# Performance work log

Measured on AMD Instinct MI355X. Metric: run time of the kernel, lower is better.

Reference implementation:

```python
import jax, jax.numpy as jnp
import numpy as np

V = 32000        # vocab_size
OOV = 100        # max_oovs
VT = V + OOV
E = 256          # embed_size
H = 256          # hidden_size
PAD_INDEX = 0


def _gru_cell(x, h, w_ih, w_hh, b_ih, b_hh):
    # PyTorch GRU gate order: r, z, n
    gi = x @ w_ih.T + b_ih
    gh = h @ w_hh.T + b_hh
    ir, iz, inn = jnp.split(gi, 3, axis=-1)
    hr, hz, hn = jnp.split(gh, 3, axis=-1)
    r = jax.nn.sigmoid(ir + hr)
    z = jax.nn.sigmoid(iz + hz)
    n = jnp.tanh(inn + r * hn)
    return (1.0 - z) * n + z * h


def setup_inputs() -> dict:
    key = jax.random.key(0)
    ks = jax.random.split(key, 16)
    bs, max_len, seq_len = 32, 64, 128
    inputs = jax.random.randint(ks[0], (bs, max_len), 0, V, dtype=jnp.int32)
    encoded = jax.random.normal(ks[1], (bs, seq_len, 2 * H), dtype=jnp.float32)
    encoded_idx = jax.random.randint(ks[2], (bs, seq_len), 0, VT, dtype=jnp.int32)
    s = 0.02
    return {
        "inputs": inputs,
        "encoded": encoded,
        "encoded_idx": encoded_idx,
        "bridge_w": s * jax.random.normal(ks[3], (H, 2 * H), dtype=jnp.float32),
        "embed": s * jax.random.normal(ks[4], (V, E), dtype=jnp.float32),
        "gru_w_ih": s * jax.random.normal(ks[5], (3 * H, E + 2 * H), dtype=jnp.float32),
        "gru_w_hh": s * jax.random.normal(ks[6], (3 * H, H), dtype=jnp.float32),
        "gru_b_ih": jnp.zeros((3 * H,), dtype=jnp.float32),
        "gru_b_hh": jnp.zeros((3 * H,), dtype=jnp.float32),
        "Wg_w": s * jax.random.normal(ks[7], (V, H), dtype=jnp.float32),
        "Wg_b": jnp.zeros((V,), dtype=jnp.float32),
        "Wo_w": s * jax.random.normal(ks[8], (H, 2 * H), dtype=jnp.float32),
        "Wo_b": jnp.zeros((H,), dtype=jnp.float32),
    }


def decoder_forward(inputs, encoded, encoded_idx, bridge_w, embed,
                    gru_w_ih, gru_w_hh, gru_b_ih, gru_b_hh,
                    Wg_w, Wg_b, Wo_w, Wo_b):
    bs, seq_len, _ = encoded.shape
    # precomputed per-sequence quantities (as in original forward())
    enc_scores = jnp.tanh(encoded @ Wo_w.T + Wo_b)            # [bs, seq, H]
    pad_mask = jnp.where(encoded_idx == PAD_INDEX, -1000.0, 0.0)  # [bs, seq]
    b_idx = jnp.arange(bs)[:, None]

    s0 = encoded[:, -1, :] @ bridge_w.T                        # [bs, H]
    ctx0 = jnp.zeros((bs, 2 * H), dtype=encoded.dtype)

    def step(carry, inp):
        s_prev, ctx = carry
        x = embed[inp]                                         # [bs, E]
        gru_in = jnp.concatenate([x, ctx], axis=-1)            # [bs, E+2H]
        s_t = _gru_cell(gru_in, s_prev, gru_w_ih, gru_w_hh, gru_b_ih, gru_b_hh)
        psi_g = s_t @ Wg_w.T + Wg_b                            # [bs, V]
        psi_c = jnp.einsum('bsh,bh->bs', enc_scores, s_t) + pad_mask
        p = jax.nn.softmax(jnp.concatenate([psi_g, psi_c], axis=1), axis=1)
        prob_g = jnp.concatenate(
            [p[:, :V], jnp.full((bs, OOV), 1e-4, dtype=p.dtype)], axis=1)  # [bs, VT]
        prob_c = p[:, V:]                                      # [bs, seq]
        # scatter-add of copy probs onto extended vocab (one-hot bmm in original)
        prob_c_to_g = jnp.zeros((bs, VT), dtype=p.dtype).at[b_idx, encoded_idx].add(prob_c)
        out = prob_g + prob_c_to_g                             # [bs, VT]
        # selective read: reweight copy probs at positions matching current input
        rel = (encoded_idx == inp[:, None]).astype(p.dtype)
        cw = rel * prob_c
        cw = cw / jnp.maximum(cw.sum(axis=1, keepdims=True), 1e-12)  # F.normalize p=1
        new_ctx = jnp.einsum('bs,bsd->bd', cw, encoded)        # [bs, 2H]
        return (s_t, new_ctx), out

    (_, _), outs = jax.lax.scan(step, (s0, ctx0), inputs.T)    # [max_len, bs, VT]
    return jnp.transpose(outs, (1, 0, 2))                      # [bs, max_len, VT]


def reference(inputs, encoded, encoded_idx, bridge_w, embed,
              gru_w_ih, gru_w_hh, gru_b_ih, gru_b_hh,
              Wg_w, Wg_b, Wo_w, Wo_b):
    return decoder_forward(inputs, encoded, encoded_idx, bridge_w, embed,
                           gru_w_ih, gru_w_hh, gru_b_ih, gru_b_hh,
                           Wg_w, Wg_b, Wo_w, Wo_b)
```

## Files before the change

### kernel.cpp

```cpp
#include <hip/hip_runtime.h>
#include <math.h>
#include <stdint.h>

static const int VOC  = 32000;
static const int VT_  = 32100;

typedef __attribute__((ext_vector_type(8))) short bf16x8_t;
typedef __attribute__((ext_vector_type(4))) float f32x4_t;

__device__ __forceinline__ unsigned short f2bf(float f) {
  union { float f; unsigned int u; } v; v.f = f;
  unsigned int u = v.u;
  u = u + 0x7FFFu + ((u >> 16) & 1u);
  return (unsigned short)(u >> 16);
}
__device__ __forceinline__ float bf2f(unsigned short u) {
  union { unsigned int i; float f; } w; w.i = ((unsigned int)u) << 16; return w.f;
}
__device__ __forceinline__ float bfbits(unsigned int u) {
  union { unsigned int i; float f; } w; w.i = u; return w.f;
}
__device__ __forceinline__ int nth_set(unsigned long long m0, unsigned long long m1, int j) {
  int c0 = __popcll(m0);
  unsigned long long m = m0; int base = 0;
  if (j >= c0) { j -= c0; m = m1; base = 64; }
  for (int k = 0; k < j; k++) m &= m - 1;
  return base + (__ffsll((long long)m) - 1);
}

__global__ __launch_bounds__(256) void k_pre0(
    const float* __restrict__ wg, unsigned short* __restrict__ WG16,
    const float* __restrict__ whh, unsigned short* __restrict__ WHH16,
    const float* __restrict__ enc, unsigned short* __restrict__ EH,
    unsigned short* __restrict__ EL,
    const float* __restrict__ wo, unsigned short* __restrict__ WOH,
    unsigned short* __restrict__ WOL,
    const float* __restrict__ wih, unsigned short* __restrict__ WIH16,
    const float* __restrict__ embed, const int* __restrict__ inputs,
    unsigned short* __restrict__ X16) {
  int q = blockIdx.x, tid = threadIdx.x;
  if (q < 1024) {
    for (int i = q * 256 + tid; i < 2048000; i += 1024 * 256) {
      float4 f = ((const float4*)wg)[i];
      ushort4 o;
      o.x = f2bf(f.x); o.y = f2bf(f.y); o.z = f2bf(f.z); o.w = f2bf(f.w);
      ((ushort4*)WG16)[i] = o;
    }
  } else if (q < 1036) {
    for (int i = (q - 1024) * 256 + tid; i < 49152; i += 12 * 256) {
      float4 f = ((const float4*)whh)[i];
      ushort4 o;
      o.x = f2bf(f.x); o.y = f2bf(f.y); o.z = f2bf(f.z); o.w = f2bf(f.w);
      ((ushort4*)WHH16)[i] = o;
    }
  } else if (q < 1292) {
    for (int i = (q - 1036) * 256 + tid; i < 524288; i += 256 * 256) {
      float4 f = ((const float4*)enc)[i];
      ushort4 h, l;
      h.x = f2bf(f.x); l.x = f2bf(f.x - bf2f(h.x));
      h.y = f2bf(f.y); l.y = f2bf(f.y - bf2f(h.y));
      h.z = f2bf(f.z); l.z = f2bf(f.z - bf2f(h.z));
      h.w = f2bf(f.w); l.w = f2bf(f.w - bf2f(h.w));
      ((ushort4*)EH)[i] = h;
      ((ushort4*)EL)[i] = l;
    }
  } else if (q < 1300) {
    for (int i = (q - 1292) * 256 + tid; i < 32768; i += 8 * 256) {
      float4 f = ((const float4*)wo)[i];
      ushort4 h, l;
      h.x = f2bf(f.x); l.x = f2bf(f.x - bf2f(h.x));
      h.y = f2bf(f.y); l.y = f2bf(f.y - bf2f(h.y));
      h.z = f2bf(f.z); l.z = f2bf(f.z - bf2f(h.z));
      h.w = f2bf(f.w); l.w = f2bf(f.w - bf2f(h.w));
      ((ushort4*)WOH)[i] = h;
      ((ushort4*)WOL)[i] = l;
    }
  } else if (q < 1312) {
    for (int g = (q - 1300) * 256 + tid; g < 49152; g += 12 * 256) {
      int row = g >> 6, col = g & 63;
      float4 f = ((const float4*)(wih + (size_t)row * 768))[col];
      ushort4 o;
      o.x = f2bf(f.x); o.y = f2bf(f.y); o.z = f2bf(f.z); o.w = f2bf(f.w);
      ((ushort4*)X16)[0];
      ((ushort4*)WIH16)[g] = o;
    }
  } else {
    for (int g = (q - 1312) * 256 + tid; g < 131072; g += 128 * 256) {
      int r = g >> 6, col = g & 63;
      float4 f = ((const float4*)(embed + (size_t)inputs[r] * 256))[col];
      ushort4 o;
      o.x = f2bf(f.x); o.y = f2bf(f.y); o.z = f2bf(f.z); o.w = f2bf(f.w);
      ((ushort4*)X16)[g] = o;
    }
  }
}

__global__ __launch_bounds__(256) void k_pre1(
    const unsigned short* __restrict__ EH, const unsigned short* __restrict__ EL,
    const unsigned short* __restrict__ WOH, const unsigned short* __restrict__ WOL,
    const float* __restrict__ wob, float* __restrict__ ENCSC,
    const unsigned short* __restrict__ X16, const unsigned short* __restrict__ WIH16,
    const float* __restrict__ bih, float* __restrict__ XG,
    const float* __restrict__ enc, const float* __restrict__ bridge,
    float* __restrict__ S0,
    const float* __restrict__ wih, const int* __restrict__ encidx,
    const int* __restrict__ inputs, float* __restrict__ ENCIH) {
  __shared__ int flag;
  int q = blockIdx.x, tid = threadIdx.x;
  int wid = tid >> 6, lane = tid & 63;
  int wm = wid >> 1, wn = wid & 1;
  int quad = lane >> 4, l15 = lane & 15;
  if (q < 256) {
    int bm = q >> 2, bn = q & 3;
    int r0 = bm * 64 + wm * 32, n0 = bn * 64 + wn * 32;
    f32x4_t acc[2][2];
#pragma unroll
    for (int i = 0; i < 2; i++)
#pragma unroll
      for (int j = 0; j < 2; j++) acc[i][j] = (f32x4_t){0.f, 0.f, 0.f, 0.f};
    for (int kc = 0; kc < 16; kc++) {
      int ko = kc * 32 + quad * 8;
      bf16x8_t ah[2], al[2], bh[2], bl[2];
#pragma unroll
      for (int i = 0; i < 2; i++) {
        size_t off = (size_t)(r0 + i * 16 + l15) * 512 + ko;
        ah[i] = *(const bf16x8_t*)(EH + off);
        al[i] = *(const bf16x8_t*)(EL + off);
      }
#pragma unroll
      for (int j = 0; j < 2; j++) {
        size_t off = (size_t)(n0 + j * 16 + l15) * 512 + ko;
        bh[j] = *(const bf16x8_t*)(WOH + off);
        bl[j] = *(const bf16x8_t*)(WOL + off);
      }
#pragma unroll
      for (int i = 0; i < 2; i++)
#pragma unroll
        for (int j = 0; j < 2; j++) {
          acc[i][j] = __builtin_amdgcn_mfma_f32_16x16x32_bf16(ah[i], bh[j], acc[i][j], 0, 0, 0);
          acc[i][j] = __builtin_amdgcn_mfma_f32_16x16x32_bf16(ah[i], bl[j], acc[i][j], 0, 0, 0);
          acc[i][j] = __builtin_amdgcn_mfma_f32_16x16x32_bf16(al[i], bh[j], acc[i][j], 0, 0, 0);
        }
    }
#pragma unroll
    for (int i = 0; i < 2; i++)
#pragma unroll
      for (int j = 0; j < 2; j++)
#pragma unroll
        for (int p = 0; p < 4; p++) {
          int row = r0 + i * 16 + quad * 4 + p;
          int col = n0 + j * 16 + l15;
          ENCSC[(size_t)row * 256 + col] = tanhf(acc[i][j][p] + wob[col]);
        }
  } else if (q < 640) {
    int p2 = q - 256;
    int bm = p2 & 31, bn = p2 >> 5;
    int r0 = bm * 64 + wm * 32, n0 = bn * 64 + wn * 32;
    f32x4_t acc[2][2];
#pragma unroll
    for (int i = 0; i < 2; i++)
#pragma unroll
      for (int j = 0; j < 2; j++) acc[i][j] = (f32x4_t){0.f, 0.f, 0.f, 0.f};
    for (int kc = 0; kc < 8; kc++) {
      int ko = kc * 32 + quad * 8;
      bf16x8_t a[2], b[2];
#pragma unroll
      for (int i = 0; i < 2; i++)
        a[i] = *(const bf16x8_t*)(X16 + (size_t)(r0 + i * 16 + l15) * 256 + ko);
#pragma unroll
      for (int j = 0; j < 2; j++)
        b[j] = *(const bf16x8_t*)(WIH16 + (size_t)(n0 + j * 16 + l15) * 256 + ko);
#pragma unroll
      for (int i = 0; i < 2; i++)
#pragma unroll
        for (int j = 0; j < 2; j++)
          acc[i][j] = __builtin_amdgcn_mfma_f32_16x16x32_bf16(a[i], b[j], acc[i][j], 0, 0, 0);
    }
#pragma unroll
    for (int i = 0; i < 2; i++)
#pragma unroll
      for (int j = 0; j < 2; j++)
#pragma unroll
        for (int p = 0; p < 4; p++) {
          int row = r0 + i * 16 + quad * 4 + p;
          int col = n0 + j * 16 + l15;
          XG[(size_t)row * 768 + col] = acc[i][j][p] + bih[col];
        }
  } else if (q < 672) {
    int b = q - 640, h = tid;
    const float4* a4 = (const float4*)(enc + ((size_t)b * 128 + 127) * 512);
    const float4* w4 = (const float4*)(bridge + (size_t)h * 512);
    float acc = 0.f;
    for (int k = 0; k < 128; k++) {
      float4 a = a4[k], w = w4[k];
      acc += a.x * w.x + a.y * w.y + a.z * w.z + a.w * w.w;
    }
    S0[b * 256 + h] = acc;
  } else {
    int bs = q - 672;
    int b = bs >> 7;
    int idx = encidx[bs];
    if (tid < 64) {
      unsigned long long m = __ballot(inputs[b * 64 + tid] == idx);
      if (tid == 0) flag = (m != 0ULL);
    }
    __syncthreads();
    if (!flag) return;
    const float4* e4 = (const float4*)(enc + (size_t)bs * 512);
    for (int d = tid; d < 768; d += 256) {
      const float4* w4 = (const float4*)(wih + (size_t)d * 768 + 256);
      float acc = 0.f;
      for (int k = 0; k < 128; k++) {
        float4 e = e4[k], w = w4[k];
        acc += e.x * w.x + e.y * w.y + e.z * w.z + e.w * w.w;
      }
      ENCIH[(size_t)bs * 768 + d] = acc;
    }
  }
}

__global__ __launch_bounds__(768, 1) void k_seq(
    const unsigned short* __restrict__ whb,
    const float* __restrict__ bhh,
    const float* __restrict__ xg, const float* __restrict__ encsc,
    const float* __restrict__ encih, const int* __restrict__ encidx,
    const int* __restrict__ inputs, const float* __restrict__ s0,
    float* __restrict__ S32, unsigned short* __restrict__ S16) {
  __shared__ float sbuf[256];
  __shared__ __align__(16) unsigned short sb16[256];
  __shared__ float ghp[768];
  __shared__ float psis[128];
  __shared__ int eidx_sh[128];
  __shared__ int inp_sh[64];
  __shared__ unsigned long long mmask[64][2];
  __shared__ __align__(16) unsigned short wlds[73728];
  int b = blockIdx.x;
  int tid = threadIdx.x;
  int wid = tid >> 6, lane = tid & 63;
  int quad = lane >> 4, l15 = lane & 15;
  int n0 = wid * 64;
  int h = tid;
#pragma unroll
  for (int c = 0; c < 4; c++)
#pragma unroll
    for (int kt2 = 0; kt2 < 3; kt2++) {
      int4 v = *(const int4*)(whb + (size_t)(n0 + c * 16 + l15) * 256 + 160 + kt2 * 32 + quad * 8);
      *(int4*)(wlds + wid * 6144 + (c * 3 + kt2) * 512 + (l15 * 4 + quad) * 8) = v;
    }
  bf16x8_t wf[20];
#pragma unroll
  for (int c = 0; c < 4; c++)
#pragma unroll
    for (int kt = 0; kt < 5; kt++)
      wf[c * 5 + kt] = *(const bf16x8_t*)(whb + (size_t)(n0 + c * 16 + l15) * 256 + kt * 32 + quad * 8);
  float bR = 0.f, bZ = 0.f, bN = 0.f, ctxR = 0.f, ctxZ = 0.f, ctxN = 0.f;
  if (tid < 256) {
    bR = bhh[h]; bZ = bhh[256 + h]; bN = bhh[512 + h];
    float v = s0[b * 256 + tid];
    sbuf[tid] = v;
    sb16[tid] = f2bf(v);
  }
  if (tid < 128) eidx_sh[tid] = encidx[b * 128 + tid];
  if (tid < 64) inp_sh[tid] = inputs[b * 64 + tid];
  __syncthreads();
  if (tid < 128) {
    int e = eidx_sh[tid];
    for (int t = 0; t < 64; t++) {
      unsigned long long bal = __ballot(e == inp_sh[t]);
      if (lane == 0) mmask[t][wid] = bal;
    }
  }
  __syncthreads();
  for (int t = 0; t < 64; t++) {
    int r = b * 64 + t;
    float xr0 = 0.f, xr1 = 0.f, xr2 = 0.f;
    if (tid < 256) {
      const float* xr = xg + (size_t)r * 768;
      xr0 = xr[h]; xr1 = xr[256 + h]; xr2 = xr[512 + h];
    }
    f32x4_t a0 = {0.f,0.f,0.f,0.f}, a1 = {0.f,0.f,0.f,0.f};
    f32x4_t a2 = {0.f,0.f,0.f,0.f}, a3 = {0.f,0.f,0.f,0.f};
#pragma unroll
    for (int kt = 0; kt < 5; kt++) {
      bf16x8_t af = *(const bf16x8_t*)(sb16 + kt * 32 + quad * 8);
      a0 = __builtin_amdgcn_mfma_f32_16x16x32_bf16(af, wf[ 0 + kt], a0, 0, 0, 0);
      a1 = __builtin_amdgcn_mfma_f32_16x16x32_bf16(af, wf[ 5 + kt], a1, 0, 0, 0);
      a2 = __builtin_amdgcn_mfma_f32_16x16x32_bf16(af, wf[10 + kt], a2, 0, 0, 0);
      a3 = __builtin_amdgcn_mfma_f32_16x16x32_bf16(af, wf[15 + kt], a3, 0, 0, 0);
    }
#pragma unroll
    for (int kt2 = 0; kt2 < 3; kt2++) {
      bf16x8_t af = *(const bf16x8_t*)(sb16 + (5 + kt2) * 32 + quad * 8);
      const unsigned short* wb = wlds + wid * 6144 + kt2 * 512 + (l15 * 4 + quad) * 8;
      a0 = __builtin_amdgcn_mfma_f32_16x16x32_bf16(af, *(const bf16x8_t*)(wb +    0), a0, 0, 0, 0);
      a1 = __builtin_amdgcn_mfma_f32_16x16x32_bf16(af, *(const bf16x8_t*)(wb + 1536), a1, 0, 0, 0);
      a2 = __builtin_amdgcn_mfma_f32_16x16x32_bf16(af, *(const bf16x8_t*)(wb + 3072), a2, 0, 0, 0);
      a3 = __builtin_amdgcn_mfma_f32_16x16x32_bf16(af, *(const bf16x8_t*)(wb + 4608), a3, 0, 0, 0);
    }
    if (lane < 16) {
      ghp[n0 +      lane] = a0[0];
      ghp[n0 + 16 + lane] = a1[0];
      ghp[n0 + 32 + lane] = a2[0];
      ghp[n0 + 48 + lane] = a3[0];
    }
    __syncthreads();
    if (tid < 256) {
      float hr = ghp[h] + bR;
      float hz = ghp[256 + h] + bZ;
      float hn = ghp[512 + h] + bN;
      float gr = xr0 + ctxR;
      float gz = xr1 + ctxZ;
      float gn = xr2 + ctxN;
      float rgate = 1.f / (1.f + expf(-(gr + hr)));
      float zgate = 1.f / (1.f + expf(-(gz + hz)));
      float ngate = tanhf(gn + rgate * hn);
      float sold = sbuf[h];
      float snew = (1.f - zgate) * ngate + zgate * sold;
      unsigned short u16 = f2bf(snew);
      S32[(size_t)r * 256 + h] = snew;
      S16[(size_t)r * 256 + h] = u16;
      sbuf[h] = snew;
      sb16[h] = u16;
    }
    __syncthreads();
    if (t == 63) break;
    unsigned long long m0 = mmask[t][0], m1 = mmask[t][1];
    int mc = __popcll(m0) + __popcll(m1);
    if (mc > 0) {
      for (int j = wid; j < mc; j += 12) {
        int s = nth_set(m0, m1, j);
        const float4* e4 = (const float4*)(encsc + (size_t)(b * 128 + s) * 256);
        float4 ev = e4[lane];
        float4 sv = ((const float4*)sbuf)[lane];
        float v = ev.x * sv.x + ev.y * sv.y + ev.z * sv.z + ev.w * sv.w;
#pragma unroll
        for (int off = 32; off >= 1; off >>= 1) v += __shfl_down(v, off);
        if (lane == 0) psis[j] = v + (eidx_sh[s] == 0 ? -1000.f : 0.f);
      }
      __syncthreads();
      if (tid == 0) {
        float mx = -3e38f;
        for (int j = 0; j < mc; j++) mx = fmaxf(mx, psis[j]);
        if (mx < -500.f) {
          for (int j = 0; j < mc; j++) psis[j] = 0.f;
        } else {
          float ss = 0.f;
          for (int j = 0; j < mc; j++) { float e = expf(psis[j] - mx); psis[j] = e; ss += e; }
          float rs = 1.f / ss;
          for (int j = 0; j < mc; j++) psis[j] *= rs;
        }
      }
      __syncthreads();
      if (tid < 256) {
        ctxR = 0.f; ctxZ = 0.f; ctxN = 0.f;
        unsigned long long mm0 = m0, mm1 = m1;
        for (int j = 0; j < mc; j++) {
          int s;
          if (mm0) { s = __ffsll((long long)mm0) - 1; mm0 &= mm0 - 1; }
          else     { s = 64 + __ffsll((long long)mm1) - 1; mm1 &= mm1 - 1; }
          float c = psis[j];
          const float* e = encih + (size_t)(b * 128 + s) * 768;
          ctxR += c * e[h]; ctxZ += c * e[256 + h]; ctxN += c * e[512 + h];
        }
      }
    } else if (tid < 256) {
      ctxR = 0.f; ctxZ = 0.f; ctxN = 0.f;
    }
  }
}

__global__ __launch_bounds__(256) void k_mid(const unsigned short* __restrict__ S16,
                                             const unsigned short* __restrict__ WG16,
                                             const float* __restrict__ wgb,
                                             unsigned short* __restrict__ pe16,
                                             const float* __restrict__ S32,
                                             const float* __restrict__ encsc,
                                             const int* __restrict__ encidx,
                                             float* __restrict__ psic) {
  int q = blockIdx.x;
  int tid = threadIdx.x;
  if (q >= 250) {
    int q2 = q - 250;
    int b = q2 >> 1, ny = q2 & 1;
    int ti = tid & 15, tj = tid >> 4;
    int r0 = b * 64 + ti * 4;
    int s0 = ny * 64 + tj * 4;
    const float4* A[4]; const float4* B[4];
#pragma unroll
    for (int i = 0; i < 4; i++) A[i] = (const float4*)(S32 + (size_t)(r0 + i) * 256);
#pragma unroll
    for (int j = 0; j < 4; j++) B[j] = (const float4*)(encsc + (size_t)(b * 128 + s0 + j) * 256);
    float acc[4][4];
#pragma unroll
    for (int i = 0; i < 4; i++)
#pragma unroll
      for (int j = 0; j < 4; j++) acc[i][j] = 0.f;
    for (int k = 0; k < 64; k++) {
      float4 a[4], bb[4];
#pragma unroll
      for (int i = 0; i < 4; i++) a[i] = A[i][k];
#pragma unroll
      for (int j = 0; j < 4; j++) bb[j] = B[j][k];
#pragma unroll
      for (int i = 0; i < 4; i++)
#pragma unroll
        for (int j = 0; j < 4; j++)
          acc[i][j] += a[i].x * bb[j].x + a[i].y * bb[j].y + a[i].z * bb[j].z + a[i].w * bb[j].w;
    }
#pragma unroll
    for (int i = 0; i < 4; i++)
#pragma unroll
      for (int j = 0; j < 4; j++) {
        float v = acc[i][j] + (encidx[b * 128 + s0 + j] == 0 ? -1000.f : 0.f);
        psic[(size_t)(r0 + i) * 128 + s0 + j] = v;
      }
    return;
  }
  __shared__ unsigned short lB[128 * 256];
  __shared__ unsigned short lA[128 * 256];
  int nc = q;
  int wid = tid >> 6, lane = tid & 63;
  int wm = wid >> 1, wn = wid & 1;
  int quad = lane >> 4, l15 = lane & 15;
#pragma unroll
  for (int u = 0; u < 16; u++) {
    int c = u * 256 + tid;
    int row = c >> 5, ch = c & 31;
    int sch = (ch & 24) | ((ch & 7) ^ (row & 7));
    __builtin_amdgcn_global_load_lds(
        (const __attribute__((address_space(1))) unsigned int*)(WG16 + (size_t)(nc * 128 + row) * 256 + sch * 8),
        (__attribute__((address_space(3))) unsigned int*)(lB + c * 8), 16, 0, 0);
  }
  float bj[4];
#pragma unroll
  for (int j = 0; j < 4; j++) bj[j] = wgb[nc * 128 + wn * 64 + j * 16 + l15];
  for (int mt = 0; mt < 16; mt++) {
#pragma unroll
    for (int u = 0; u < 16; u++) {
      int c = u * 256 + tid;
      int row = c >> 5, ch = c & 31;
      int sch = (ch & 24) | ((ch & 7) ^ (row & 7));
      __builtin_amdgcn_global_load_lds(
          (const __attribute__((address_space(1))) unsigned int*)(S16 + (size_t)(mt * 128 + row) * 256 + sch * 8),
          (__attribute__((address_space(3))) unsigned int*)(lA + c * 8), 16, 0, 0);
    }
    __syncthreads();
    f32x4_t acc[4][4];
#pragma unroll
    for (int i = 0; i < 4; i++)
#pragma unroll
      for (int j = 0; j < 4; j++) acc[i][j] = (f32x4_t){0.f, 0.f, 0.f, 0.f};
#pragma unroll
    for (int kc = 0; kc < 8; kc++) {
      int g = kc * 4 + quad;
      int slotoff = ((g & 24) | ((g & 7) ^ (l15 & 7))) * 8;
      bf16x8_t af[4], bfr[4];
#pragma unroll
      for (int i = 0; i < 4; i++)
        af[i] = *(const bf16x8_t*)(lA + (wm * 64 + i * 16 + l15) * 256 + slotoff);
#pragma unroll
      for (int j = 0; j < 4; j++)
        bfr[j] = *(const bf16x8_t*)(lB + (wn * 64 + j * 16 + l15) * 256 + slotoff);
#pragma unroll
      for (int i = 0; i < 4; i++)
#pragma unroll
        for (int j = 0; j < 4; j++)
          acc[i][j] = __builtin_amdgcn_mfma_f32_16x16x32_bf16(af[i], bfr[j], acc[i][j], 0, 0, 0);
    }
#pragma unroll
    for (int i = 0; i < 4; i++)
#pragma unroll
      for (int p = 0; p < 4; p++) {
        int rg = mt * 128 + wm * 64 + i * 16 + quad * 4 + p;
        size_t base = (size_t)rg * 32000 + nc * 128 + wn * 64 + l15;
#pragma unroll
        for (int j = 0; j < 4; j++)
          pe16[base + j * 16] = f2bf(expf(acc[i][j][p] + bj[j]));
      }
    __syncthreads();
  }
}

__global__ __launch_bounds__(256) void k_pb(const unsigned short* __restrict__ pe16,
                                            const float* __restrict__ psic,
                                            const int* __restrict__ encidx,
                                            float* __restrict__ outp) {
  __shared__ float red[8];
  int r = blockIdx.x;
  int b = r >> 6;
  int tid = threadIdx.x;
  int wid = tid >> 6, lane = tid & 63;
  const unsigned short* prow = pe16 + (size_t)r * 32000;
  float* orow = outp + (size_t)r * VT_;
  int4 ev[16];
#pragma unroll
  for (int u = 0; u < 16; u++) {
    int c8 = u * 256 + tid;
    if (c8 < 4000) ev[u] = *(const int4*)(prow + c8 * 8);
    else ev[u] = (int4){0, 0, 0, 0};
  }
  float sumE = 0.f;
#pragma unroll
  for (int u = 0; u < 16; u++) {
    unsigned int xs0 = (unsigned int)ev[u].x, xs1 = (unsigned int)ev[u].y;
    unsigned int xs2 = (unsigned int)ev[u].z, xs3 = (unsigned int)ev[u].w;
    sumE += bfbits(xs0 << 16) + bfbits(xs0 & 0xffff0000u);
    sumE += bfbits(xs1 << 16) + bfbits(xs1 & 0xffff0000u);
    sumE += bfbits(xs2 << 16) + bfbits(xs2 & 0xffff0000u);
    sumE += bfbits(xs3 << 16) + bfbits(xs3 & 0xffff0000u);
  }
  float t = sumE;
#pragma unroll
  for (int off = 32; off >= 1; off >>= 1) t += __shfl_xor(t, off);
  if (lane == 0) red[wid] = t;
  float pc = (tid < 128) ? psic[(size_t)r * 128 + tid] : -3e38f;
  float mv = pc;
#pragma unroll
  for (int off = 32; off >= 1; off >>= 1) mv = fmaxf(mv, __shfl_xor(mv, off));
  if (lane == 0) red[4 + wid] = mv;
  __syncthreads();
  float sumEt = red[0] + red[1] + red[2] + red[3];
  float Mc = fmaxf(fmaxf(red[4], red[5]), fmaxf(red[6], red[7]));
  float D = fmaxf(Mc - 30.f, 0.f);
  float w = expf(-D);
  __syncthreads();
  float ec = (tid < 128) ? expf(pc - D) : 0.f;
  float zt = ec;
#pragma unroll
  for (int off = 32; off >= 1; off >>= 1) zt += __shfl_xor(zt, off);
  if (lane == 0) red[wid] = zt;
  __syncthreads();
  float Z = w * sumEt + (red[0] + red[1] + red[2] + red[3]);
  float gs = w / Z;
#pragma unroll 2
  for (int u = 0; u < 16; u++) {
    int c8 = u * 256 + tid;
    if (c8 < 4000) {
      int c0 = c8 * 8;
      unsigned int xs0 = (unsigned int)ev[u].x, xs1 = (unsigned int)ev[u].y;
      unsigned int xs2 = (unsigned int)ev[u].z, xs3 = (unsigned int)ev[u].w;
      float4 o0, o1;
      o0.x = bfbits(xs0 << 16) * gs;         o0.y = bfbits(xs0 & 0xffff0000u) * gs;
      o0.z = bfbits(xs1 << 16) * gs;         o0.w = bfbits(xs1 & 0xffff0000u) * gs;
      o1.x = bfbits(xs2 << 16) * gs;         o1.y = bfbits(xs2 & 0xffff0000u) * gs;
      o1.z = bfbits(xs3 << 16) * gs;         o1.w = bfbits(xs3 & 0xffff0000u) * gs;
      *(float4*)(orow + c0) = o0;
      *(float4*)(orow + c0 + 4) = o1;
    }
  }
  if (tid < 100) orow[32000 + tid] = 1e-4f;
  __syncthreads();
  if (tid < 128) {
    int idx = encidx[b * 128 + tid];
    atomicAdd(&orow[idx], ec / Z);
  }
}

extern "C" void kernel_launch(void* const* d_in, const int* in_sizes, int n_in,
                              void* d_out, int out_size, void* d_ws, size_t ws_size,
                              hipStream_t stream) {
  (void)in_sizes; (void)n_in; (void)out_size; (void)ws_size;
  const int*   inputs  = (const int*)d_in[0];
  const float* encoded = (const float*)d_in[1];
  const int*   encidx  = (const int*)d_in[2];
  const float* bridge  = (const float*)d_in[3];
  const float* embed   = (const float*)d_in[4];
  const float* wih     = (const float*)d_in[5];
  const float* whh     = (const float*)d_in[6];
  const float* bih     = (const float*)d_in[7];
  const float* bhh     = (const float*)d_in[8];
  const float* wg      = (const float*)d_in[9];
  const float* wgb     = (const float*)d_in[10];
  const float* wo      = (const float*)d_in[11];
  const float* wob     = (const float*)d_in[12];
  float* out = (float*)d_out;

  char* ws = (char*)d_ws;
  size_t off = 0;
  auto alloc = [&](size_t bytes) -> void* {
    void* p = ws + off;
    off += (bytes + 255) & ~(size_t)255;
    return p;
  };
  unsigned short* WG16  = (unsigned short*)alloc((size_t)32000 * 256 * 2);
  unsigned short* WHH16 = (unsigned short*)alloc((size_t)768 * 256 * 2);
  unsigned short* EH    = (unsigned short*)alloc((size_t)4096 * 512 * 2);
  unsigned short* EL    = (unsigned short*)alloc((size_t)4096 * 512 * 2);
  unsigned short* WOH   = (unsigned short*)alloc((size_t)256 * 512 * 2);
  unsigned short* WOL   = (unsigned short*)alloc((size_t)256 * 512 * 2);
  unsigned short* WIH16 = (unsigned short*)alloc((size_t)768 * 256 * 2);
  unsigned short* X16   = (unsigned short*)alloc((size_t)2048 * 256 * 2);
  float* S32            = (float*)alloc((size_t)2048 * 256 * 4);
  unsigned short* S16   = (unsigned short*)alloc((size_t)2048 * 256 * 2);
  float* ENCSC          = (float*)alloc((size_t)4096 * 256 * 4);
  float* ENCIH          = (float*)alloc((size_t)4096 * 768 * 4);
  float* XG             = (float*)alloc((size_t)2048 * 768 * 4);
  float* S0             = (float*)alloc((size_t)32 * 256 * 4);
  float* PSIC           = (float*)alloc((size_t)2048 * 128 * 4);
  unsigned short* PE16  = (unsigned short*)alloc((size_t)2048 * 32000 * 2);

  k_pre0<<<1440, 256, 0, stream>>>(wg, WG16, whh, WHH16, encoded, EH, EL,
                                   wo, WOH, WOL, wih, WIH16, embed, inputs, X16);
  k_pre1<<<4768, 256, 0, stream>>>(EH, EL, WOH, WOL, wob, ENCSC,
                                   X16, WIH16, bih, XG,
                                   encoded, bridge, S0, wih, encidx, inputs, ENCIH);
  k_seq<<<32, 768, 0, stream>>>(WHH16, bhh, XG, ENCSC, ENCIH, encidx, inputs, S0, S32, S16);
  k_mid<<<314, 256, 0, stream>>>(S16, WG16, wgb, PE16, S32, ENCSC, encidx, PSIC);
  k_pb<<<2048, 256, 0, stream>>>(PE16, PSIC, encidx, out);
}
```

Baseline: 776.2 us.

## Fuse softmax row-sum partials into vocab GEMM epilogue, drop register-held row in k_pb

The vocab projection kernel now sums the bf16-rounded exp values per row tile with cross-lane shuffles and shared memory, and writes per-(row, column-block) partial sums to a new buffer. The normalisation kernel reduces those 250 partials instead of reading and summing the whole 32000-entry bf16 row before the scaling pass. It then loads the row only once, inside the scale loop, so the 16 int4 values no longer have to be held in registers. This adds shuffles, one shared-memory write and a block barrier per tile in the GEMM epilogue, plus a small extra global buffer.

```diff
diff --git a/kernel.cpp b/kernel.cpp
--- a/kernel.cpp
+++ b/kernel.cpp
@@ -81,7 +81,6 @@
       float4 f = ((const float4*)(wih + (size_t)row * 768))[col];
       ushort4 o;
       o.x = f2bf(f.x); o.y = f2bf(f.y); o.z = f2bf(f.z); o.w = f2bf(f.w);
-      ((ushort4*)X16)[0];
       ((ushort4*)WIH16)[g] = o;
     }
   } else {
@@ -373,6 +372,7 @@
                                              const unsigned short* __restrict__ WG16,
                                              const float* __restrict__ wgb,
                                              unsigned short* __restrict__ pe16,
+                                             float* __restrict__ psum,
                                              const float* __restrict__ S32,
                                              const float* __restrict__ encsc,
                                              const int* __restrict__ encidx,
@@ -418,6 +418,7 @@
   }
   __shared__ unsigned short lB[128 * 256];
   __shared__ unsigned short lA[128 * 256];
+  __shared__ float zpart[2][128];
   int nc = q;
   int wid = tid >> 6, lane = tid & 63;
   int wm = wid >> 1, wn = wid & 1;
@@ -471,17 +472,28 @@
     for (int i = 0; i < 4; i++)
 #pragma unroll
       for (int p = 0; p < 4; p++) {
-        int rg = mt * 128 + wm * 64 + i * 16 + quad * 4 + p;
+        int rl = wm * 64 + i * 16 + quad * 4 + p;
+        int rg = mt * 128 + rl;
         size_t base = (size_t)rg * 32000 + nc * 128 + wn * 64 + l15;
-#pragma unroll
-        for (int j = 0; j < 4; j++)
-          pe16[base + j * 16] = f2bf(expf(acc[i][j][p] + bj[j]));
+        float rs = 0.f;
+#pragma unroll
+        for (int j = 0; j < 4; j++) {
+          unsigned short us = f2bf(expf(acc[i][j][p] + bj[j]));
+          pe16[base + j * 16] = us;
+          rs += bf2f(us);
+        }
+#pragma unroll
+        for (int off = 1; off < 16; off <<= 1) rs += __shfl_xor(rs, off);
+        if (l15 == 0) zpart[wn][rl] = rs;
       }
     __syncthreads();
+    if (tid < 128)
+      psum[(size_t)(mt * 128 + tid) * 256 + nc] = zpart[0][tid] + zpart[1][tid];
   }
 }
 
 __global__ __launch_bounds__(256) void k_pb(const unsigned short* __restrict__ pe16,
+                                            const float* __restrict__ psum,
                                             const float* __restrict__ psic,
                                             const int* __restrict__ encidx,
                                             float* __restrict__ outp) {
@@ -492,27 +504,10 @@
   int wid = tid >> 6, lane = tid & 63;
   const unsigned short* prow = pe16 + (size_t)r * 32000;
   float* orow = outp + (size_t)r * VT_;
-  int4 ev[16];
-#pragma unroll
-  for (int u = 0; u < 16; u++) {
-    int c8 = u * 256 + tid;
-    if (c8 < 4000) ev[u] = *(const int4*)(prow + c8 * 8);
-    else ev[u] = (int4){0, 0, 0, 0};
-  }
-  float sumE = 0.f;
-#pragma unroll
-  for (int u = 0; u < 16; u++) {
-    unsigned int xs0 = (unsigned int)ev[u].x, xs1 = (unsigned int)ev[u].y;
-    unsigned int xs2 = (unsigned int)ev[u].z, xs3 = (unsigned int)ev[u].w;
-    sumE += bfbits(xs0 << 16) + bfbits(xs0 & 0xffff0000u);
-    sumE += bfbits(xs1 << 16) + bfbits(xs1 & 0xffff0000u);
-    sumE += bfbits(xs2 << 16) + bfbits(xs2 & 0xffff0000u);
-    sumE += bfbits(xs3 << 16) + bfbits(xs3 & 0xffff0000u);
-  }
-  float t = sumE;
-#pragma unroll
-  for (int off = 32; off >= 1; off >>= 1) t += __shfl_xor(t, off);
-  if (lane == 0) red[wid] = t;
+  float zp = (tid < 250) ? psum[(size_t)r * 256 + tid] : 0.f;
+#pragma unroll
+  for (int off = 32; off >= 1; off >>= 1) zp += __shfl_xor(zp, off);
+  if (lane == 0) red[wid] = zp;
   float pc = (tid < 128) ? psic[(size_t)r * 128 + tid] : -3e38f;
   float mv = pc;
 #pragma unroll
@@ -532,13 +527,13 @@
   __syncthreads();
   float Z = w * sumEt + (red[0] + red[1] + red[2] + red[3]);
   float gs = w / Z;
-#pragma unroll 2
   for (int u = 0; u < 16; u++) {
     int c8 = u * 256 + tid;
     if (c8 < 4000) {
       int c0 = c8 * 8;
-      unsigned int xs0 = (unsigned int)ev[u].x, xs1 = (unsigned int)ev[u].y;
-      unsigned int xs2 = (unsigned int)ev[u].z, xs3 = (unsigned int)ev[u].w;
+      int4 v = *(const int4*)(prow + c0);
+      unsigned int xs0 = (unsigned int)v.x, xs1 = (unsigned int)v.y;
+      unsigned int xs2 = (unsigned int)v.z, xs3 = (unsigned int)v.w;
       float4 o0, o1;
       o0.x = bfbits(xs0 << 16) * gs;         o0.y = bfbits(xs0 & 0xffff0000u) * gs;
       o0.z = bfbits(xs1 << 16) * gs;         o0.w = bfbits(xs1 & 0xffff0000u) * gs;
@@ -597,6 +592,7 @@
   float* XG             = (float*)alloc((size_t)2048 * 768 * 4);
   float* S0             = (float*)alloc((size_t)32 * 256 * 4);
   float* PSIC           = (float*)alloc((size_t)2048 * 128 * 4);
+  float* PSUM           = (float*)alloc((size_t)2048 * 256 * 4);
   unsigned short* PE16  = (unsigned short*)alloc((size_t)2048 * 32000 * 2);
 
   k_pre0<<<1440, 256, 0, stream>>>(wg, WG16, whh, WHH16, encoded, EH, EL,
@@ -605,6 +601,6 @@
                                    X16, WIH16, bih, XG,
                                    encoded, bridge, S0, wih, encidx, inputs, ENCIH);
   k_seq<<<32, 768, 0, stream>>>(WHH16, bhh, XG, ENCSC, ENCIH, encidx, inputs, S0, S32, S16);
-  k_mid<<<314, 256, 0, stream>>>(S16, WG16, wgb, PE16, S32, ENCSC, encidx, PSIC);
-  k_pb<<<2048, 256, 0, stream>>>(PE16, PSIC, encidx, out);
-}
+  k_mid<<<314, 256, 0, stream>>>(S16, WG16, wgb, PE16, PSUM, S32, ENCSC, encidx, PSIC);
+  k_pb<<<2048, 256, 0, stream>>>(PE16, PSUM, PSIC, encidx, out);
+}
```

New measurement: 751.7 us. 3.2% less time.
